# Kernel optimization log

Measured on AMD Instinct MI355X. Metric: run time of the kernel, lower is better.

Reference implementation:

```python
import jax, jax.numpy as jnp
import numpy as np

B, C_IN, C_OUT, K, H, W = 32, 128, 256, 3, 56, 56
STRIDE, PAD = 1, 1


def setup_inputs() -> dict:
    key = jax.random.key(0)
    kx, kw, kb = jax.random.split(key, 3)
    x = jax.random.normal(kx, (B, C_IN, H, W), dtype=jnp.float32)
    weight = jax.random.normal(kw, (C_OUT, C_IN, K, K), dtype=jnp.float32)
    bias = jax.random.normal(kb, (C_OUT,), dtype=jnp.float32)
    return {"x": x, "weight": weight, "bias": bias}


def reference(x, weight, bias):
    # Binarize weights to {-1, 0, +1} exactly like torch.sign
    w_bin = jnp.sign(weight)
    out = jax.lax.conv_general_dilated(
        x, w_bin,
        window_strides=(STRIDE, STRIDE),
        padding=[(PAD, PAD), (PAD, PAD)],
        dimension_numbers=("NCHW", "OIHW", "NCHW"),
    )
    return out + bias[None, :, None, None]
```

## Files before the change

### kernel.cpp

```cpp
#include <hip/hip_runtime.h>
#include <cstdint>
#include <cstddef>

typedef _Float16 f16;
typedef _Float16 f16x4 __attribute__((ext_vector_type(4)));
typedef _Float16 f16x8 __attribute__((ext_vector_type(8)));
typedef float    f32x4 __attribute__((ext_vector_type(4)));

#define CIN    128
#define COUT   256
#define HH     56
#define WW     56
#define HW     3136
#define PPDIM  3364
#define XPLANE (PPDIM*CIN)

__device__ __forceinline__ void gload16(const void* g, void* l) {
  __builtin_amdgcn_global_load_lds((const __attribute__((address_space(1))) unsigned int*)g,
                                   (__attribute__((address_space(3))) unsigned int*)l,
                                   16, 0, 0);
}

__global__ __launch_bounds__(256) void xpad_kernel(const float* __restrict__ x,
                                                   f16* __restrict__ xp) {
  const int bid = blockIdx.x;
  const int pr  = bid % 58;
  const int b   = bid / 58;
  const int tid = threadIdx.x;
  __shared__ f16 tile[128 * 65];

  const bool interior = (pr >= 1) && (pr <= 56);
  if (interior) {
    const int h = pr - 1;
    #pragma unroll
    for (int it = 0; it < 7; ++it) {
      int i  = it * 256 + tid;
      int c  = i / 14;
      int wq = i - c * 14;
      const float* src = x + (((size_t)(b * CIN + c) * HH + h) * WW + wq * 4);
      f32x4 v = *(const f32x4*)src;
      f16x4 t = { (f16)v.x, (f16)v.y, (f16)v.z, (f16)v.w };
      *(f16x4*)&tile[c * 65 + wq * 4] = t;
    }
  }
  __syncthreads();
  f16* orow = xp + (size_t)b * XPLANE + (size_t)pr * 58 * CIN;
  for (int i = tid; i < 928; i += 256) {
    int px = i >> 4;
    int cg = i & 15;
    f16x8 v = {};
    if (interior && px >= 1 && px <= 56) {
      int w = px - 1;
      #pragma unroll
      for (int j = 0; j < 8; ++j) v[j] = tile[(cg * 8 + j) * 65 + w];
    }
    *(f16x8*)(orow + (size_t)px * CIN + cg * 8) = v;
  }
}

__global__ __launch_bounds__(256) void wprep_kernel(const float* __restrict__ w,
                                                    f16* __restrict__ wt) {
  int t = blockIdx.x * 256 + threadIdx.x;
  int s     = t >> 14;
  int hidx  = t & 16383;
  int co    = hidx >> 6;
  int khalf = (hidx & 63) ^ ((co & 4) << 2);
  int kidx  = s >> 1;
  int c     = ((s & 1) << 6) + khalf;
  float v = w[(size_t)co * 1152 + c * 9 + kidx];
  wt[t] = (f16)((v > 0.f) ? 1.f : (v < 0.f ? -1.f : 0.f));
}

__global__ __launch_bounds__(512) void bconv_main(
    const f16* __restrict__ xp, const f16* __restrict__ wt,
    const float* __restrict__ bias, float* __restrict__ out) {
  __shared__ __align__(16) f16 Alds[128 * 64];
  __shared__ __align__(16) f16 Blds[256 * 64];
  const int tid = threadIdx.x;
  const int p0  = blockIdx.x * 128;

  const int wave = tid >> 6, lane = tid & 63;
  const int pxl  = tid >> 3;
  const int kx_s = ((tid & 7) << 4) ^ ((pxl & 4) << 3);
  const int pga  = p0 + pxl;
  const int pgb  = pga + 64;
  const int ba = pga / HW, ra = pga % HW;
  const int bb = pgb / HW, rb = pgb % HW;
  const int ha = ra / WW, wa = ra % WW;
  const int hb = rb / WW, wb = rb % WW;
  const char* xpB = (const char*)xp;
  const char* srcA0 = xpB + 2 * ((size_t)ba * XPLANE + (size_t)((ha + 1) * 58 + wa + 1) * CIN) + kx_s;
  const char* srcA1 = xpB + 2 * ((size_t)bb * XPLANE + (size_t)((hb + 1) * 58 + wb + 1) * CIN) + kx_s;
  char* AldsB = (char*)Alds;
  char* BldsB = (char*)Blds;
  char* dstA0 = AldsB + (wave << 10);
  char* dstA1 = AldsB + 8192 + (wave << 10);
  const char* wtB = (const char*)wt + (tid << 4);
  char* dstB = BldsB + (wave << 10);

  const int wpx = wave >> 2;
  const int wco = wave & 3;
  const int l15 = lane & 15, l4 = lane >> 4;
  const int kxr = (l15 & 4) << 3;
  const int rA = ((wpx << 6) + l15) << 7;
  const int rB = ((wco << 6) + l15) << 7;

  f32x4 acc[4][4];
  #pragma unroll
  for (int i = 0; i < 4; ++i)
    #pragma unroll
    for (int j = 0; j < 4; ++j) acc[i][j] = (f32x4){0.f, 0.f, 0.f, 0.f};

  #pragma unroll 1
  for (int s = 0; s < 18; ++s) {
    const int kidx = s >> 1, ch = s & 1;
    const int dh = kidx / 3 - 1, dw = kidx - (kidx / 3) * 3 - 1;
    const long toff = (long)(dh * 58 + dw) * 256 + ch * 128;
    gload16(srcA0 + toff, dstA0);
    gload16(srcA1 + toff, dstA1);
    const char* ws = wtB + (size_t)s * 32768;
    gload16(ws,         dstB);
    gload16(ws + 8192,  dstB + 8192);
    gload16(ws + 16384, dstB + 16384);
    gload16(ws + 24576, dstB + 24576);
    __syncthreads();

    #pragma unroll
    for (int kk = 0; kk < 2; ++kk) {
      const int ko = ((kk << 6) + (l4 << 4)) ^ kxr;
      f16x8 xf[4], wf[4];
      #pragma unroll
      for (int j = 0; j < 4; ++j)
        xf[j] = *(const f16x8*)(AldsB + rA + (j << 11) + ko);
      #pragma unroll
      for (int i = 0; i < 4; ++i)
        wf[i] = *(const f16x8*)(BldsB + rB + (i << 11) + ko);
      #pragma unroll
      for (int i = 0; i < 4; ++i)
        #pragma unroll
        for (int j = 0; j < 4; ++j)
          acc[i][j] = __builtin_amdgcn_mfma_f32_16x16x32_f16(wf[i], xf[j], acc[i][j], 0, 0, 0);
    }
    __syncthreads();
  }

  #pragma unroll
  for (int j = 0; j < 4; ++j) {
    const int pg = p0 + wpx * 64 + j * 16 + l15;
    const int bo = pg / HW;
    const int pr = pg % HW;
    float* ob = out + (size_t)bo * (COUT * HW) + pr;
    #pragma unroll
    for (int i = 0; i < 4; ++i) {
      const int cb2 = wco * 64 + i * 16 + l4 * 4;
      #pragma unroll
      for (int r = 0; r < 4; ++r) {
        const int co = cb2 + r;
        ob[(size_t)co * HW] = acc[i][j][r] + bias[co];
      }
    }
  }
}

extern "C" void kernel_launch(void* const* d_in, const int* in_sizes, int n_in,
                              void* d_out, int out_size, void* d_ws, size_t ws_size,
                              hipStream_t stream) {
  const float* x    = (const float*)d_in[0];
  const float* w    = (const float*)d_in[1];
  const float* bias = (const float*)d_in[2];
  float* out = (float*)d_out;

  f16* xp = (f16*)d_ws;
  f16* wt = xp + (size_t)32 * XPLANE;

  xpad_kernel<<<1856, 256, 0, stream>>>(x, xp);
  wprep_kernel<<<1152, 256, 0, stream>>>(w, wt);
  bconv_main<<<784, 512, 0, stream>>>(xp, wt, bias, out);
}
```

Before: 207.0 us.

## Widen LDS XOR swizzle and rewrite pad kernel without shared-memory transpose

The LDS swizzle for the A and B tiles now XORs with three row bits at 16-byte granularity instead of one bit, which should spread the ds_read fragments across more banks and cut LDS bank conflicts in the MFMA loop. The weight prep swizzle is changed to match. Separately, the input pad/transpose kernel drops its shared-memory tile: each lane reads strided channels for one pixel and writes 8-channel f16 vectors directly, and the border rows and columns are zero-filled explicitly. That removes a barrier and LDS traffic, but the global reads become strided across channels, so they coalesce only across lanes within a row.

```diff
diff --git a/kernel.cpp b/kernel.cpp
--- a/kernel.cpp
+++ b/kernel.cpp
@@ -27,34 +27,32 @@
   const int pr  = bid % 58;
   const int b   = bid / 58;
   const int tid = threadIdx.x;
-  __shared__ f16 tile[128 * 65];
+  f16* orow = xp + (size_t)b * XPLANE + (size_t)pr * 58 * CIN;
 
-  const bool interior = (pr >= 1) && (pr <= 56);
-  if (interior) {
-    const int h = pr - 1;
+  if (pr == 0 || pr == 57) {
+    for (int i = tid; i < 928; i += 256)
+      *(f16x8*)(orow + (size_t)i * 8) = (f16x8){};
+    return;
+  }
+  const int h = pr - 1;
+  const int wave = tid >> 6, lane = tid & 63;
+  if (tid < 32) {
+    int px = (tid < 16) ? 0 : 57;
+    int cg = tid & 15;
+    *(f16x8*)(orow + (size_t)px * CIN + cg * 8) = (f16x8){};
+  }
+  if (lane < 56) {
+    const float* xb = x + (size_t)b * CIN * HW + (size_t)h * WW + lane;
+    f16* op = orow + (size_t)(lane + 1) * CIN;
     #pragma unroll
-    for (int it = 0; it < 7; ++it) {
-      int i  = it * 256 + tid;
-      int c  = i / 14;
-      int wq = i - c * 14;
-      const float* src = x + (((size_t)(b * CIN + c) * HH + h) * WW + wq * 4);
-      f32x4 v = *(const f32x4*)src;
-      f16x4 t = { (f16)v.x, (f16)v.y, (f16)v.z, (f16)v.w };
-      *(f16x4*)&tile[c * 65 + wq * 4] = t;
+    for (int cg = 0; cg < 4; ++cg) {
+      const int c0 = (wave * 4 + cg) * 8;
+      f16x8 v;
+      #pragma unroll
+      for (int j = 0; j < 8; ++j)
+        v[j] = (f16)xb[(size_t)(c0 + j) * HW];
+      *(f16x8*)(op + c0) = v;
     }
-  }
-  __syncthreads();
-  f16* orow = xp + (size_t)b * XPLANE + (size_t)pr * 58 * CIN;
-  for (int i = tid; i < 928; i += 256) {
-    int px = i >> 4;
-    int cg = i & 15;
-    f16x8 v = {};
-    if (interior && px >= 1 && px <= 56) {
-      int w = px - 1;
-      #pragma unroll
-      for (int j = 0; j < 8; ++j) v[j] = tile[(cg * 8 + j) * 65 + w];
-    }
-    *(f16x8*)(orow + (size_t)px * CIN + cg * 8) = v;
   }
 }
 
@@ -64,7 +62,7 @@
   int s     = t >> 14;
   int hidx  = t & 16383;
   int co    = hidx >> 6;
-  int khalf = (hidx & 63) ^ ((co & 4) << 2);
+  int khalf = (hidx & 63) ^ ((co & 7) << 3);
   int kidx  = s >> 1;
   int c     = ((s & 1) << 6) + khalf;
   float v = w[(size_t)co * 1152 + c * 9 + kidx];
@@ -81,7 +79,7 @@
 
   const int wave = tid >> 6, lane = tid & 63;
   const int pxl  = tid >> 3;
-  const int kx_s = ((tid & 7) << 4) ^ ((pxl & 4) << 3);
+  const int kx_s = ((tid & 7) << 4) ^ ((pxl & 7) << 4);
   const int pga  = p0 + pxl;
   const int pgb  = pga + 64;
   const int ba = pga / HW, ra = pga % HW;
@@ -101,7 +99,7 @@
   const int wpx = wave >> 2;
   const int wco = wave & 3;
   const int l15 = lane & 15, l4 = lane >> 4;
-  const int kxr = (l15 & 4) << 3;
+  const int kxr = (l15 & 7) << 4;
   const int rA = ((wpx << 6) + l15) << 7;
   const int rB = ((wco << 6) + l15) << 7;
 
```

Measured after the change: 210.3 us. No clear change (+1.6%).
